# Optimization experiments

Hardware: AMD Instinct MI355X
Metric: run time of the kernel (lower is better)

Reference implementation:

```python
import jax, jax.numpy as jnp
import numpy as np
from jax import lax

B, T, D, H = 64, 2048, 128, 256

def _lstm_layer(x, Wih, Whh, bih, bhh):
    # x: [B, T, in]; Wih: [4H, in]; Whh: [4H, H]
    xp = jnp.einsum('bti,gi->btg', x, Wih) + bih + bhh  # [B, T, 4H]
    h0 = jnp.zeros((x.shape[0], Whh.shape[1]), x.dtype)
    c0 = jnp.zeros_like(h0)
    def step(carry, xt):
        h, c = carry
        g = xt + h @ Whh.T
        i, f, gg, o = jnp.split(g, 4, axis=-1)
        c = jax.nn.sigmoid(f) * c + jax.nn.sigmoid(i) * jnp.tanh(gg)
        h = jax.nn.sigmoid(o) * jnp.tanh(c)
        return (h, c), h
    _, hs = lax.scan(step, (h0, c0), jnp.swapaxes(xp, 0, 1))  # hs: [T, B, H]
    return jnp.swapaxes(hs, 0, 1)

def setup_inputs() -> dict:
    key = jax.random.key(0)
    ks = jax.random.split(key, 16)
    s_ih0 = 1.0 / np.sqrt(H)
    inp = {
        'x': jax.random.normal(ks[0], (B, T, D), jnp.float32),
        'Wih0': jax.random.uniform(ks[1], (4 * H, D), jnp.float32, -s_ih0, s_ih0),
        'Whh0': jax.random.uniform(ks[2], (4 * H, H), jnp.float32, -s_ih0, s_ih0),
        'bih0': jax.random.uniform(ks[3], (4 * H,), jnp.float32, -s_ih0, s_ih0),
        'bhh0': jax.random.uniform(ks[4], (4 * H,), jnp.float32, -s_ih0, s_ih0),
        'Wih1': jax.random.uniform(ks[5], (4 * H, H), jnp.float32, -s_ih0, s_ih0),
        'Whh1': jax.random.uniform(ks[6], (4 * H, H), jnp.float32, -s_ih0, s_ih0),
        'bih1': jax.random.uniform(ks[7], (4 * H,), jnp.float32, -s_ih0, s_ih0),
        'bhh1': jax.random.uniform(ks[8], (4 * H,), jnp.float32, -s_ih0, s_ih0),
        'attn_W1': jax.random.normal(ks[9], (H, H), jnp.float32) * np.sqrt(2.0 / (H + H)),
        'attn_W2': jax.random.normal(ks[10], (H, H), jnp.float32) * np.sqrt(2.0 / (H + H)),
        'attn_w': jax.random.uniform(ks[11], (H,), jnp.float32, -0.1, 0.1),
        'ln_gamma': jnp.ones((H,), jnp.float32),
        'ln_beta': jnp.zeros((H,), jnp.float32),
    }
    return inp

def reference(x, Wih0, Whh0, bih0, bhh0, Wih1, Whh1, bih1, bhh1, attn_W1, attn_W2, attn_w, ln_gamma, ln_beta):
    h1 = _lstm_layer(x, Wih0, Whh0, bih0, bhh0)       # [B, T, H]
    lstm_out = _lstm_layer(h1, Wih1, Whh1, bih1, bhh1)  # [B, T, H]
    h_T = lstm_out[:, -1, :]                            # [B, H]
    # vectorized additive attention over all timesteps
    alpha = jnp.tanh(jnp.einsum('bth,hk->btk', lstm_out, attn_W1)
                     + (h_T @ attn_W2)[:, None, :])     # [B, T, H]
    scores = alpha @ attn_w                             # [B, T]
    w = jax.nn.softmax(scores, axis=1)
    context = jnp.einsum('bt,bth->bh', w, lstm_out)     # [B, H]
    mu = jnp.mean(context, axis=-1, keepdims=True)
    var = jnp.var(context, axis=-1, keepdims=True)
    out = (context - mu) / jnp.sqrt(var + 1e-5) * ln_gamma + ln_beta
    return out
```

## Files before the change

### kernel.cpp

```cpp
#include <hip/hip_runtime.h>
#include <hip/hip_bf16.h>
#include <math.h>

#define B 64
#define T 2048
#define D 128
#define H 256
#define G 1024

#define L0_UINTS 49152
#define L1_UINTS 65536
#define PQ_UINTS (L0_UINTS + L1_UINTS)

#define L0_RES 22
#define L1_RES 20
#define L0_LDS 2
#define L1_LDS 12

typedef _Float16 h2v __attribute__((ext_vector_type(2)));
typedef float f2v __attribute__((ext_vector_type(2)));
typedef unsigned int u4v __attribute__((ext_vector_type(4)));

#if defined(__has_builtin)
#if __has_builtin(__builtin_amdgcn_fdot2)
#define HAS_FDOT2 1
#endif
#endif

__device__ __forceinline__ float dot2(unsigned int w, unsigned int h, float acc) {
#ifdef HAS_FDOT2
    return __builtin_amdgcn_fdot2(__builtin_bit_cast(h2v, w), __builtin_bit_cast(h2v, h), acc, false);
#else
    h2v wv = __builtin_bit_cast(h2v, w);
    h2v hv = __builtin_bit_cast(h2v, h);
    acc = fmaf((float)wv.x, (float)hv.x, acc);
    return fmaf((float)wv.y, (float)hv.y, acc);
#endif
}

__device__ __forceinline__ unsigned short f2h(float f) {
    _Float16 h = (_Float16)f;
    return __builtin_bit_cast(unsigned short, h);
}
__device__ __forceinline__ float h2f(unsigned short u) {
    return (float)__builtin_bit_cast(_Float16, u);
}
__device__ __forceinline__ unsigned int packh2(float a, float b) {
    return (unsigned int)f2h(a) | ((unsigned int)f2h(b) << 16);
}
__device__ __forceinline__ float sigm(float x) { return 1.0f / (1.0f + __expf(-x)); }
__device__ __forceinline__ float ftanh(float x) {
    x = fminf(fmaxf(x, -15.0f), 15.0f);
    float e = __expf(2.0f * x);
    return (e - 1.0f) / (e + 1.0f);
}

#define DOT4(w0, hp, a0, a1, a2, a3) \
    a0 = dot2(w0.x, hp, a0); a1 = dot2(w0.y, hp, a1); a2 = dot2(w0.z, hp, a2); a3 = dot2(w0.w, hp, a3);

__global__ void k_zero(unsigned int* p, int n) {
    int i = blockIdx.x * blockDim.x + threadIdx.x;
    if (i < n) p[i] = 0u;
}

__global__ void k_bias_sum(const float* __restrict__ a, const float* __restrict__ b,
                           float* __restrict__ out, int n) {
    int i = blockIdx.x * blockDim.x + threadIdx.x;
    if (i < n) out[i] = a[i] + b[i];
}

__global__ void k_pack_w(const float* __restrict__ Wih0, const float* __restrict__ Whh0,
                         const float* __restrict__ Wih1, const float* __restrict__ Whh1,
                         unsigned int* __restrict__ PW) {
    int idx = blockIdx.x * blockDim.x + threadIdx.x;
    if (idx >= 4 * PQ_UINTS) return;
    int q = idx / PQ_UINTS;
    int off = idx % PQ_UINTS;
    float v0, v1;
    if (off < L0_UINTS) {
        int kp = off >> 8, c = off & 255;
        int gate = c >> 6, u = c & 63;
        int r = gate * 256 + q * 64 + u;
        int k = kp * 2;
        if (k < 128) { v0 = Wih0[(size_t)r * 128 + k];       v1 = Wih0[(size_t)r * 128 + k + 1]; }
        else         { v0 = Whh0[(size_t)r * 256 + k - 128]; v1 = Whh0[(size_t)r * 256 + k - 127]; }
    } else {
        int o2 = off - L0_UINTS;
        int kp = o2 >> 8, c = o2 & 255;
        int gate = c >> 6, u = c & 63;
        int r = gate * 256 + q * 64 + u;
        int k = kp * 2;
        if (k < 256) { v0 = Wih1[(size_t)r * 256 + k];       v1 = Wih1[(size_t)r * 256 + k + 1]; }
        else         { v0 = Whh1[(size_t)r * 256 + k - 256]; v1 = Whh1[(size_t)r * 256 + k - 255]; }
    }
    PW[idx] = packh2(v0, v1);
}

__global__ __launch_bounds__(1024, 4) void k_lstm_split(
    const float* __restrict__ x,
    const unsigned int* __restrict__ PW,
    const float* __restrict__ bs0,
    const float* __restrict__ bs1,
    unsigned int* __restrict__ hxq,
    unsigned int* __restrict__ flags,
    unsigned int* __restrict__ seqo)
{
    __shared__ float s_gacc[8][512];
    __shared__ float s_g[512];
    __shared__ unsigned int s_k0p[192];
    __shared__ unsigned int s_k1p[256];
    __shared__ uint4 wl0[L0_LDS][512];
    __shared__ uint4 wl1[L1_LDS][512];

    const int q   = blockIdx.x >> 6;
    const int b   = blockIdx.x & 63;
    const int tid = threadIdx.x;
    const int half = tid >> 9;
    const int t2  = tid & 511;
    const int cg  = t2 & 63;
    const int kb  = t2 >> 6;

    const unsigned int* Wq = PW + (size_t)q * PQ_UINTS;
    const unsigned int* wbase =
        half == 0 ? (Wq + (size_t)(kb * 24) * 256 + 4 * cg)
                  : (Wq + L0_UINTS + (size_t)(kb * 32) * 256 + 4 * cg);

    uint4 wr[L0_RES];
    if (half == 0) {
        #pragma unroll
        for (int i = 0; i < L0_RES; ++i) wr[i] = *(const uint4*)(wbase + (size_t)i * 256);
        #pragma unroll
        for (int c = 0; c < L0_LDS; ++c)
            wl0[c][t2] = *(const uint4*)(wbase + (size_t)(L0_RES + c) * 256);
    } else {
        #pragma unroll
        for (int i = 0; i < L1_RES; ++i) wr[i] = *(const uint4*)(wbase + (size_t)i * 256);
        #pragma unroll
        for (int c = 0; c < L1_LDS; ++c)
            wl1[c][t2] = *(const uint4*)(wbase + (size_t)(L1_RES + c) * 256);
    }

    float bi0 = 0.f, bi1 = 0.f, bi2 = 0.f, bi3 = 0.f;
    if (tid < 64) {
        int u = q * 64 + tid;
        bi0 = bs0[u]; bi1 = bs0[256 + u]; bi2 = bs0[512 + u]; bi3 = bs0[768 + u];
    } else if (tid < 128) {
        int u = q * 64 + (tid - 64);
        bi0 = bs1[u]; bi1 = bs1[256 + u]; bi2 = bs1[512 + u]; bi3 = bs1[768 + u];
    }
    float c0 = 0.f, c1 = 0.f;
    unsigned int hb0 = 0u, hb1 = 0u, hb2 = 0u, hb3 = 0u;

    if (tid < 128) s_k0p[64 + tid] = 0u;
    if (tid >= 128 && tid < 384) s_k1p[tid - 128] = 0u;
    if (tid >= 384 && tid < 448) {
        int i = tid - 384;
        f2v v = __builtin_nontemporal_load((const f2v*)(x + (size_t)b * T * D) + i);
        s_k0p[i] = packh2(v.x, v.y);
    }

    for (int t = 0; ; ++t) {
        __syncthreads();

        if (half == 0) {
            if (t < T) {
                const unsigned int* sp = s_k0p + kb * 24;
                float a0 = 0.f, a1 = 0.f, a2 = 0.f, a3 = 0.f;
                #pragma unroll
                for (int i = 0; i < 5; ++i) {
                    uint4 hp = *(const uint4*)(sp + 4 * i);
                    DOT4(wr[4 * i + 0], hp.x, a0, a1, a2, a3);
                    DOT4(wr[4 * i + 1], hp.y, a0, a1, a2, a3);
                    DOT4(wr[4 * i + 2], hp.z, a0, a1, a2, a3);
                    DOT4(wr[4 * i + 3], hp.w, a0, a1, a2, a3);
                }
                {
                    uint4 hp = *(const uint4*)(sp + 20);
                    DOT4(wr[20], hp.x, a0, a1, a2, a3);
                    DOT4(wr[21], hp.y, a0, a1, a2, a3);
                    uint4 wa = wl0[0][t2];
                    DOT4(wa, hp.z, a0, a1, a2, a3);
                    uint4 wb = wl0[1][t2];
                    DOT4(wb, hp.w, a0, a1, a2, a3);
                }
                *(float4*)&s_gacc[kb][4 * cg] = make_float4(a0, a1, a2, a3);
            }
        } else {
            const unsigned int* sp = s_k1p + kb * 32;
            float a0 = 0.f, a1 = 0.f, a2 = 0.f, a3 = 0.f;
            #pragma unroll
            for (int i = 0; i < 5; ++i) {
                uint4 hp = *(const uint4*)(sp + 4 * i);
                DOT4(wr[4 * i + 0], hp.x, a0, a1, a2, a3);
                DOT4(wr[4 * i + 1], hp.y, a0, a1, a2, a3);
                DOT4(wr[4 * i + 2], hp.z, a0, a1, a2, a3);
                DOT4(wr[4 * i + 3], hp.w, a0, a1, a2, a3);
            }
            #pragma unroll
            for (int g = 0; g < 3; ++g) {
                uint4 hp = *(const uint4*)(sp + 20 + 4 * g);
                uint4 w0 = wl1[4 * g + 0][t2];
                DOT4(w0, hp.x, a0, a1, a2, a3);
                uint4 w1 = wl1[4 * g + 1][t2];
                DOT4(w1, hp.y, a0, a1, a2, a3);
                uint4 w2 = wl1[4 * g + 2][t2];
                DOT4(w2, hp.z, a0, a1, a2, a3);
                uint4 w3 = wl1[4 * g + 3][t2];
                DOT4(w3, hp.w, a0, a1, a2, a3);
            }
            *(float4*)&s_gacc[kb][256 + 4 * cg] = make_float4(a0, a1, a2, a3);
        }
        __syncthreads();

        if (tid < 512) {
            float s = s_gacc[0][tid] + s_gacc[1][tid] + s_gacc[2][tid] + s_gacc[3][tid]
                    + s_gacc[4][tid] + s_gacc[5][tid] + s_gacc[6][tid] + s_gacc[7][tid];
            s_g[tid] = s;
        }
        __syncthreads();

        if (tid < 64) {
            if (t < T) {
                int u = tid;
                float gi = s_g[u] + bi0;
                float gf = s_g[64 + u] + bi1;
                float gg = s_g[128 + u] + bi2;
                float go = s_g[192 + u] + bi3;
                c0 = sigm(gf) * c0 + sigm(gi) * ftanh(gg);
                float h0v = sigm(go) * ftanh(c0);
                float other = __shfl_xor(h0v, 1);
                if ((u & 1) == 0) {
                    __hip_atomic_store(hxq + ((((size_t)(t & 1) * 4 + q) * 64 + b) * 64) + (u >> 1),
                                       packh2(h0v, other), __ATOMIC_RELAXED, __HIP_MEMORY_SCOPE_AGENT);
                }
            }
        } else if (tid < 128) {
            int u = tid - 64;
            float h1v = 0.0f;
            if (t >= 1) {
                float gi = s_g[256 + u] + bi0;
                float gf = s_g[320 + u] + bi1;
                float gg = s_g[384 + u] + bi2;
                float go = s_g[448 + u] + bi3;
                c1 = sigm(gf) * c1 + sigm(gi) * ftanh(gg);
                h1v = sigm(go) * ftanh(c1);
                unsigned int hv = (unsigned int)f2h(h1v);
                int s = (t - 1) & 7;
                switch (s) {
                    case 0: hb0 = hv; break;
                    case 1: hb0 |= hv << 16; break;
                    case 2: hb1 = hv; break;
                    case 3: hb1 |= hv << 16; break;
                    case 4: hb2 = hv; break;
                    case 5: hb2 |= hv << 16; break;
                    case 6: hb3 = hv; break;
                    default: hb3 |= hv << 16; break;
                }
                if (s == 7) {
                    size_t idx = ((size_t)b * (T / 8) + ((t - 1) >> 3)) * H + (q * 64 + u);
                    u4v val = {hb0, hb1, hb2, hb3};
                    __builtin_nontemporal_store(val, (u4v*)(seqo + idx * 4));
                }
            }
            if (t < T) {
                float other = __shfl_xor(h1v, 1);
                if ((u & 1) == 0) {
                    __hip_atomic_store(hxq + ((((size_t)(t & 1) * 4 + q) * 64 + b) * 64) + 32 + (u >> 1),
                                       packh2(h1v, other), __ATOMIC_RELAXED, __HIP_MEMORY_SCOPE_AGENT);
                }
            }
        }

        if (t == T) break;

        __syncthreads();

        if (tid == 0) {
            __hip_atomic_store(flags + ((size_t)q * 64 + b) * 64, (unsigned)(t + 1),
                               __ATOMIC_RELAXED, __HIP_MEMORY_SCOPE_AGENT);
        }

        {
            const int wv = tid >> 6, l = tid & 63;
            if (wv < 4) {
                unsigned f = 0;
                const unsigned int* fp = flags + ((size_t)wv * 64 + b) * 64;
                do {
                    if (l == 0) f = __hip_atomic_load(fp, __ATOMIC_RELAXED, __HIP_MEMORY_SCOPE_AGENT);
                    f = __shfl(f, 0);
                    if (f < (unsigned)(t + 1)) __builtin_amdgcn_s_sleep(1);
                } while (f < (unsigned)(t + 1));
                unsigned v = __hip_atomic_load(
                    hxq + ((((size_t)(t & 1) * 4 + wv) * 64 + b) * 64) + l,
                    __ATOMIC_RELAXED, __HIP_MEMORY_SCOPE_AGENT);
                if (l < 32) {
                    s_k0p[64 + wv * 32 + l] = v;
                    s_k1p[wv * 32 + l] = v;
                } else {
                    s_k1p[128 + wv * 32 + (l - 32)] = v;
                }
            } else if (wv == 4) {
                if (t + 1 < T) {
                    f2v v = __builtin_nontemporal_load(
                        (const f2v*)(x + ((size_t)b * T + (t + 1)) * D) + l);
                    s_k0p[l] = packh2(v.x, v.y);
                }
            }
        }
    }
}

__global__ __launch_bounds__(256) void k_a2(const unsigned int* __restrict__ seq,
                                            const float* __restrict__ W2,
                                            float* __restrict__ a2out)
{
    __shared__ float s_hT[H];
    int b = blockIdx.x;
    int k = threadIdx.x;
    unsigned v = seq[(((size_t)b * (T / 8) + 255) * H + k) * 4 + 3];
    s_hT[k] = h2f((unsigned short)(v >> 16));
    __syncthreads();
    float acc = 0.f;
    #pragma unroll 4
    for (int h = 0; h < H; ++h) acc += s_hT[h] * W2[h * H + k];
    a2out[b * H + k] = acc;
}

__global__ __launch_bounds__(256) void k_scores(const unsigned int* __restrict__ seq,
                                                const float* __restrict__ W1,
                                                const float* __restrict__ a2,
                                                const float* __restrict__ attn_w,
                                                float* __restrict__ scores)
{
    const int RPB = 32;
    __shared__ float s_rows[RPB][H];
    __shared__ float s_part[RPB][4];
    int b   = blockIdx.y;
    int t0  = blockIdx.x * RPB;
    int tid = threadIdx.x;

    for (int it = tid; it < 4 * H; it += 256) {
        int tgi = it >> 8, h = it & 255;
        uint4 v = ((const uint4*)seq)[((size_t)b * (T / 8) + (t0 >> 3) + tgi) * H + h];
        int r0 = tgi * 8;
        s_rows[r0 + 0][h] = h2f((unsigned short)v.x);
        s_rows[r0 + 1][h] = h2f((unsigned short)(v.x >> 16));
        s_rows[r0 + 2][h] = h2f((unsigned short)v.y);
        s_rows[r0 + 3][h] = h2f((unsigned short)(v.y >> 16));
        s_rows[r0 + 4][h] = h2f((unsigned short)v.z);
        s_rows[r0 + 5][h] = h2f((unsigned short)(v.z >> 16));
        s_rows[r0 + 6][h] = h2f((unsigned short)v.w);
        s_rows[r0 + 7][h] = h2f((unsigned short)(v.w >> 16));
    }
    __syncthreads();

    int c = tid;
    float acc[RPB];
    #pragma unroll
    for (int r = 0; r < RPB; ++r) acc[r] = 0.f;
    for (int h = 0; h < H; ++h) {
        float w = W1[h * H + c];
        #pragma unroll
        for (int r = 0; r < RPB; ++r) acc[r] += s_rows[r][h] * w;
    }
    float a2v = a2[b * H + c];
    float wc  = attn_w[c];
    int lane = tid & 63, wv = tid >> 6;
    #pragma unroll
    for (int r = 0; r < RPB; ++r) {
        float v = ftanh(acc[r] + a2v) * wc;
        for (int off = 32; off; off >>= 1) v += __shfl_down(v, off);
        if (lane == 0) s_part[r][wv] = v;
    }
    __syncthreads();
    if (tid < RPB) {
        scores[(size_t)b * T + t0 + tid] =
            s_part[tid][0] + s_part[tid][1] + s_part[tid][2] + s_part[tid][3];
    }
}

__global__ __launch_bounds__(256) void k_finish(const unsigned int* __restrict__ seq,
                                                const float* __restrict__ scores,
                                                const float* __restrict__ gamma,
                                                const float* __restrict__ beta,
                                                float* __restrict__ out)
{
    __shared__ float s_p[T];
    __shared__ float s_red[4];
    const int b = blockIdx.x;
    const int tid = threadIdx.x;
    const int lane = tid & 63, wv = tid >> 6;

    const float* sc = scores + (size_t)b * T;
    float m = -1e30f;
    for (int t = tid; t < T; t += 256) m = fmaxf(m, sc[t]);
    for (int off = 32; off; off >>= 1) m = fmaxf(m, __shfl_down(m, off));
    if (lane == 0) s_red[wv] = m;
    __syncthreads();
    m = fmaxf(fmaxf(s_red[0], s_red[1]), fmaxf(s_red[2], s_red[3]));
    __syncthreads();

    float z = 0.f;
    for (int t = tid; t < T; t += 256) { float e = __expf(sc[t] - m); s_p[t] = e; z += e; }
    for (int off = 32; off; off >>= 1) z += __shfl_down(z, off);
    if (lane == 0) s_red[wv] = z;
    __syncthreads();
    z = s_red[0] + s_red[1] + s_red[2] + s_red[3];
    float rz = 1.0f / z;
    __syncthreads();

    const uint4* sq = (const uint4*)seq + (size_t)b * (T / 8) * H + tid;
    float ctx = 0.f;
    for (int tg = 0; tg < T / 8; ++tg) {
        uint4 v = sq[(size_t)tg * H];
        const float* pp = &s_p[tg * 8];
        ctx += pp[0] * h2f((unsigned short)v.x) + pp[1] * h2f((unsigned short)(v.x >> 16))
             + pp[2] * h2f((unsigned short)v.y) + pp[3] * h2f((unsigned short)(v.y >> 16))
             + pp[4] * h2f((unsigned short)v.z) + pp[5] * h2f((unsigned short)(v.z >> 16))
             + pp[6] * h2f((unsigned short)v.w) + pp[7] * h2f((unsigned short)(v.w >> 16));
    }
    ctx *= rz;

    float s1 = ctx;
    for (int off = 32; off; off >>= 1) s1 += __shfl_down(s1, off);
    if (lane == 0) s_red[wv] = s1;
    __syncthreads();
    float mu = (s_red[0] + s_red[1] + s_red[2] + s_red[3]) * (1.0f / H);
    __syncthreads();
    float dv = ctx - mu;
    float s2 = dv * dv;
    for (int off = 32; off; off >>= 1) s2 += __shfl_down(s2, off);
    if (lane == 0) s_red[wv] = s2;
    __syncthreads();
    float var = (s_red[0] + s_red[1] + s_red[2] + s_red[3]) * (1.0f / H);
    out[b * H + tid] = dv * rsqrtf(var + 1e-5f) * gamma[tid] + beta[tid];
}

extern "C" void kernel_launch(void* const* d_in, const int* in_sizes, int n_in,
                              void* d_out, int out_size, void* d_ws, size_t ws_size,
                              hipStream_t stream) {
    const float* x     = (const float*)d_in[0];
    const float* Wih0  = (const float*)d_in[1];
    const float* Whh0  = (const float*)d_in[2];
    const float* bih0  = (const float*)d_in[3];
    const float* bhh0  = (const float*)d_in[4];
    const float* Wih1  = (const float*)d_in[5];
    const float* Whh1  = (const float*)d_in[6];
    const float* bih1  = (const float*)d_in[7];
    const float* bhh1  = (const float*)d_in[8];
    const float* aW1   = (const float*)d_in[9];
    const float* aW2   = (const float*)d_in[10];
    const float* aw    = (const float*)d_in[11];
    const float* gamma = (const float*)d_in[12];
    const float* beta  = (const float*)d_in[13];
    float* out = (float*)d_out;

    char* base = (char*)d_ws;
    unsigned int* PW    = (unsigned int*)(base);
    float* bsum0        = (float*)(base + 1835008);
    float* bsum1        = (float*)(base + 1839104);
    unsigned int* flags = (unsigned int*)(base + 1843200);
    unsigned int* hxq   = (unsigned int*)(base + 1908736);
    float* a2buf        = (float*)(base + 2039808);
    float* scoresb      = (float*)(base + 2105344);
    unsigned int* seqo  = (unsigned int*)(base + 2629632);

    k_zero<<<(4 * 64 * 64 + 255) / 256, 256, 0, stream>>>(flags, 4 * 64 * 64);
    k_pack_w<<<(4 * PQ_UINTS) / 256, 256, 0, stream>>>(Wih0, Whh0, Wih1, Whh1, PW);
    k_bias_sum<<<(G + 255) / 256, 256, 0, stream>>>(bih0, bhh0, bsum0, G);
    k_bias_sum<<<(G + 255) / 256, 256, 0, stream>>>(bih1, bhh1, bsum1, G);

    k_lstm_split<<<256, 1024, 0, stream>>>(x, PW, bsum0, bsum1, hxq, flags, seqo);

    k_a2<<<B, H, 0, stream>>>(seqo, aW2, a2buf);
    k_scores<<<dim3(T / 32, B), 256, 0, stream>>>(seqo, aW1, a2buf, aw, scoresb);
    k_finish<<<B, 256, 0, stream>>>(seqo, scoresb, gamma, beta, out);
}
```

Measured before the change: 8.200 ms.

## Repartition persistent LSTM across 16 hidden slices times 16 batch groups

The persistent two-layer LSTM kernel changes its work split. Each block used to own a 64-unit quarter of the hidden state for one batch row. Now each block owns a 16-unit slice for a group of 4 batch rows, so every weight element loaded from LDS is reused across 4 batches. All of a slice's weights now live in LDS instead of per-thread registers, and partial sums are reduced with cross-lane shuffles. Each block now waits on 16 peer flags per step instead of 4, which adds inter-block synchronisation traffic in exchange for less register pressure and better weight reuse.

```diff
diff --git a/kernel.cpp b/kernel.cpp
--- a/kernel.cpp
+++ b/kernel.cpp
@@ -8,14 +8,13 @@
 #define H 256
 #define G 1024
 
-#define L0_UINTS 49152
-#define L1_UINTS 65536
-#define PQ_UINTS (L0_UINTS + L1_UINTS)
-
-#define L0_RES 22
-#define L1_RES 20
-#define L0_LDS 2
-#define L1_LDS 12
+#define NSL 16
+#define NB 4
+#define NG 16
+#define L0_U4 3072
+#define L1_U4 4096
+#define SL_U4 (L0_U4 + L1_U4)
+#define SL_UINTS (SL_U4 * 4)
 
 typedef _Float16 h2v __attribute__((ext_vector_type(2)));
 typedef float f2v __attribute__((ext_vector_type(2)));
@@ -55,8 +54,15 @@
     return (e - 1.0f) / (e + 1.0f);
 }
 
-#define DOT4(w0, hp, a0, a1, a2, a3) \
-    a0 = dot2(w0.x, hp, a0); a1 = dot2(w0.y, hp, a1); a2 = dot2(w0.z, hp, a2); a3 = dot2(w0.w, hp, a3);
+#define DOTB(w_, h_) \
+    A0.x=dot2(w_.x,h_.x,A0.x); A0.y=dot2(w_.x,h_.y,A0.y); A0.z=dot2(w_.x,h_.z,A0.z); A0.w=dot2(w_.x,h_.w,A0.w); \
+    A1.x=dot2(w_.y,h_.x,A1.x); A1.y=dot2(w_.y,h_.y,A1.y); A1.z=dot2(w_.y,h_.z,A1.z); A1.w=dot2(w_.y,h_.w,A1.w); \
+    A2.x=dot2(w_.z,h_.x,A2.x); A2.y=dot2(w_.z,h_.y,A2.y); A2.z=dot2(w_.z,h_.z,A2.z); A2.w=dot2(w_.z,h_.w,A2.w); \
+    A3.x=dot2(w_.w,h_.x,A3.x); A3.y=dot2(w_.w,h_.y,A3.y); A3.z=dot2(w_.w,h_.z,A3.z); A3.w=dot2(w_.w,h_.w,A3.w);
+
+#define RED4(A) \
+    A.x += __shfl_xor(A.x, 16); A.y += __shfl_xor(A.y, 16); A.z += __shfl_xor(A.z, 16); A.w += __shfl_xor(A.w, 16); \
+    A.x += __shfl_xor(A.x, 32); A.y += __shfl_xor(A.y, 32); A.z += __shfl_xor(A.z, 32); A.w += __shfl_xor(A.w, 32);
 
 __global__ void k_zero(unsigned int* p, int n) {
     int i = blockIdx.x * blockDim.x + threadIdx.x;
@@ -73,180 +79,158 @@
                          const float* __restrict__ Wih1, const float* __restrict__ Whh1,
                          unsigned int* __restrict__ PW) {
     int idx = blockIdx.x * blockDim.x + threadIdx.x;
-    if (idx >= 4 * PQ_UINTS) return;
-    int q = idx / PQ_UINTS;
-    int off = idx % PQ_UINTS;
+    if (idx >= NSL * SL_UINTS) return;
+    int s = idx / SL_UINTS;
+    int rem = idx % SL_UINTS;
     float v0, v1;
-    if (off < L0_UINTS) {
-        int kp = off >> 8, c = off & 255;
-        int gate = c >> 6, u = c & 63;
-        int r = gate * 256 + q * 64 + u;
-        int k = kp * 2;
-        if (k < 128) { v0 = Wih0[(size_t)r * 128 + k];       v1 = Wih0[(size_t)r * 128 + k + 1]; }
-        else         { v0 = Whh0[(size_t)r * 256 + k - 128]; v1 = Whh0[(size_t)r * 256 + k - 127]; }
+    if (rem < L0_U4 * 4) {
+        int q4 = rem >> 2, e = rem & 3;
+        int kb = q4 / 96; int r = q4 % 96; int kp = r >> 4; int cg = r & 15;
+        int c = cg * 4 + e; int g4 = c >> 4; int u = c & 15;
+        int row = g4 * 256 + s * 16 + u;
+        int k = (kb * 6 + kp) * 2;
+        if (k < 128) { v0 = Wih0[(size_t)row * 128 + k];         v1 = Wih0[(size_t)row * 128 + k + 1]; }
+        else         { v0 = Whh0[(size_t)row * 256 + (k - 128)]; v1 = Whh0[(size_t)row * 256 + (k - 127)]; }
     } else {
-        int o2 = off - L0_UINTS;
-        int kp = o2 >> 8, c = o2 & 255;
-        int gate = c >> 6, u = c & 63;
-        int r = gate * 256 + q * 64 + u;
-        int k = kp * 2;
-        if (k < 256) { v0 = Wih1[(size_t)r * 256 + k];       v1 = Wih1[(size_t)r * 256 + k + 1]; }
-        else         { v0 = Whh1[(size_t)r * 256 + k - 256]; v1 = Whh1[(size_t)r * 256 + k - 255]; }
+        int rem2 = rem - L0_U4 * 4;
+        int q4 = rem2 >> 2, e = rem2 & 3;
+        int kb = q4 / 128; int r = q4 % 128; int kp = r >> 4; int cg = r & 15;
+        int c = cg * 4 + e; int g4 = c >> 4; int u = c & 15;
+        int row = g4 * 256 + s * 16 + u;
+        int k = (kb * 8 + kp) * 2;
+        if (k < 256) { v0 = Wih1[(size_t)row * 256 + k];         v1 = Wih1[(size_t)row * 256 + k + 1]; }
+        else         { v0 = Whh1[(size_t)row * 256 + (k - 256)]; v1 = Whh1[(size_t)row * 256 + (k - 255)]; }
     }
     PW[idx] = packh2(v0, v1);
 }
 
-__global__ __launch_bounds__(1024, 4) void k_lstm_split(
+__global__ __launch_bounds__(1024) void k_lstm_split(
     const float* __restrict__ x,
-    const unsigned int* __restrict__ PW,
+    const uint4* __restrict__ PW2,
     const float* __restrict__ bs0,
     const float* __restrict__ bs1,
-    unsigned int* __restrict__ hxq,
+    unsigned int* __restrict__ hxg,
     unsigned int* __restrict__ flags,
     unsigned int* __restrict__ seqo)
 {
+    __shared__ uint4 wl[SL_U4];
     __shared__ float s_gacc[8][512];
     __shared__ float s_g[512];
-    __shared__ unsigned int s_k0p[192];
-    __shared__ unsigned int s_k1p[256];
-    __shared__ uint4 wl0[L0_LDS][512];
-    __shared__ uint4 wl1[L1_LDS][512];
-
-    const int q   = blockIdx.x >> 6;
-    const int b   = blockIdx.x & 63;
+    __shared__ unsigned int s_k0p[768];
+    __shared__ unsigned int s_k1p[1024];
+
+    const int g   = blockIdx.x & 15;
+    const int s   = blockIdx.x >> 4;
     const int tid = threadIdx.x;
-    const int half = tid >> 9;
-    const int t2  = tid & 511;
-    const int cg  = t2 & 63;
-    const int kb  = t2 >> 6;
-
-    const unsigned int* Wq = PW + (size_t)q * PQ_UINTS;
-    const unsigned int* wbase =
-        half == 0 ? (Wq + (size_t)(kb * 24) * 256 + 4 * cg)
-                  : (Wq + L0_UINTS + (size_t)(kb * 32) * 256 + 4 * cg);
-
-    uint4 wr[L0_RES];
-    if (half == 0) {
-        #pragma unroll
-        for (int i = 0; i < L0_RES; ++i) wr[i] = *(const uint4*)(wbase + (size_t)i * 256);
-        #pragma unroll
-        for (int c = 0; c < L0_LDS; ++c)
-            wl0[c][t2] = *(const uint4*)(wbase + (size_t)(L0_RES + c) * 256);
-    } else {
-        #pragma unroll
-        for (int i = 0; i < L1_RES; ++i) wr[i] = *(const uint4*)(wbase + (size_t)i * 256);
-        #pragma unroll
-        for (int c = 0; c < L1_LDS; ++c)
-            wl1[c][t2] = *(const uint4*)(wbase + (size_t)(L1_RES + c) * 256);
+    const int lane = tid & 63;
+    const int wv   = tid >> 6;
+    const int cg   = lane & 15;
+    const int kbs  = lane >> 4;
+
+    {
+        const uint4* PWs = PW2 + (size_t)s * SL_U4;
+        for (int i = tid; i < SL_U4; i += 1024) wl[i] = PWs[i];
     }
 
     float bi0 = 0.f, bi1 = 0.f, bi2 = 0.f, bi3 = 0.f;
     if (tid < 64) {
-        int u = q * 64 + tid;
-        bi0 = bs0[u]; bi1 = bs0[256 + u]; bi2 = bs0[512 + u]; bi3 = bs0[768 + u];
+        int u = tid >> 2;
+        bi0 = bs0[s * 16 + u]; bi1 = bs0[256 + s * 16 + u];
+        bi2 = bs0[512 + s * 16 + u]; bi3 = bs0[768 + s * 16 + u];
     } else if (tid < 128) {
-        int u = q * 64 + (tid - 64);
-        bi0 = bs1[u]; bi1 = bs1[256 + u]; bi2 = bs1[512 + u]; bi3 = bs1[768 + u];
+        int u = (tid - 64) >> 2;
+        bi0 = bs1[s * 16 + u]; bi1 = bs1[256 + s * 16 + u];
+        bi2 = bs1[512 + s * 16 + u]; bi3 = bs1[768 + s * 16 + u];
     }
     float c0 = 0.f, c1 = 0.f;
     unsigned int hb0 = 0u, hb1 = 0u, hb2 = 0u, hb3 = 0u;
 
-    if (tid < 128) s_k0p[64 + tid] = 0u;
-    if (tid >= 128 && tid < 384) s_k1p[tid - 128] = 0u;
-    if (tid >= 384 && tid < 448) {
-        int i = tid - 384;
-        f2v v = __builtin_nontemporal_load((const f2v*)(x + (size_t)b * T * D) + i);
-        s_k0p[i] = packh2(v.x, v.y);
+    if (tid < 512) s_k0p[256 + tid] = 0u;
+    s_k1p[tid] = 0u;
+    if (tid >= 512 && tid < 768) {
+        int i = tid - 512; int b = i >> 6; int kp = i & 63;
+        f2v v = __builtin_nontemporal_load((const f2v*)(x + (size_t)(g * NB + b) * T * D) + kp);
+        s_k0p[kp * 4 + b] = packh2(v.x, v.y);
     }
 
     for (int t = 0; ; ++t) {
         __syncthreads();
 
-        if (half == 0) {
+        if (wv < 8) {
             if (t < T) {
-                const unsigned int* sp = s_k0p + kb * 24;
-                float a0 = 0.f, a1 = 0.f, a2 = 0.f, a3 = 0.f;
+                int kb = wv * 4 + kbs;
+                const uint4* wp = wl + (size_t)(kb * 6) * 16 + cg;
+                float4 A0 = make_float4(0.f,0.f,0.f,0.f), A1 = A0, A2 = A0, A3 = A0;
                 #pragma unroll
-                for (int i = 0; i < 5; ++i) {
-                    uint4 hp = *(const uint4*)(sp + 4 * i);
-                    DOT4(wr[4 * i + 0], hp.x, a0, a1, a2, a3);
-                    DOT4(wr[4 * i + 1], hp.y, a0, a1, a2, a3);
-                    DOT4(wr[4 * i + 2], hp.z, a0, a1, a2, a3);
-                    DOT4(wr[4 * i + 3], hp.w, a0, a1, a2, a3);
-                }
-                {
-                    uint4 hp = *(const uint4*)(sp + 20);
-                    DOT4(wr[20], hp.x, a0, a1, a2, a3);
-                    DOT4(wr[21], hp.y, a0, a1, a2, a3);
-                    uint4 wa = wl0[0][t2];
-                    DOT4(wa, hp.z, a0, a1, a2, a3);
-                    uint4 wb = wl0[1][t2];
-                    DOT4(wb, hp.w, a0, a1, a2, a3);
-                }
-                *(float4*)&s_gacc[kb][4 * cg] = make_float4(a0, a1, a2, a3);
+                for (int kp = 0; kp < 6; ++kp) {
+                    uint4 w = wp[kp * 16];
+                    uint4 h = *(const uint4*)&s_k0p[(kb * 6 + kp) * 4];
+                    DOTB(w, h);
+                }
+                RED4(A0); RED4(A1); RED4(A2); RED4(A3);
+                if (kbs == 0) {
+                    *(float4*)&s_gacc[wv][cg * 16 + 0]  = A0;
+                    *(float4*)&s_gacc[wv][cg * 16 + 4]  = A1;
+                    *(float4*)&s_gacc[wv][cg * 16 + 8]  = A2;
+                    *(float4*)&s_gacc[wv][cg * 16 + 12] = A3;
+                }
             }
         } else {
-            const unsigned int* sp = s_k1p + kb * 32;
-            float a0 = 0.f, a1 = 0.f, a2 = 0.f, a3 = 0.f;
+            int kb = (wv - 8) * 4 + kbs;
+            const uint4* wp = wl + L0_U4 + (size_t)(kb * 8) * 16 + cg;
+            float4 A0 = make_float4(0.f,0.f,0.f,0.f), A1 = A0, A2 = A0, A3 = A0;
             #pragma unroll
-            for (int i = 0; i < 5; ++i) {
-                uint4 hp = *(const uint4*)(sp + 4 * i);
-                DOT4(wr[4 * i + 0], hp.x, a0, a1, a2, a3);
-                DOT4(wr[4 * i + 1], hp.y, a0, a1, a2, a3);
-                DOT4(wr[4 * i + 2], hp.z, a0, a1, a2, a3);
-                DOT4(wr[4 * i + 3], hp.w, a0, a1, a2, a3);
-            }
-            #pragma unroll
-            for (int g = 0; g < 3; ++g) {
-                uint4 hp = *(const uint4*)(sp + 20 + 4 * g);
-                uint4 w0 = wl1[4 * g + 0][t2];
-                DOT4(w0, hp.x, a0, a1, a2, a3);
-                uint4 w1 = wl1[4 * g + 1][t2];
-                DOT4(w1, hp.y, a0, a1, a2, a3);
-                uint4 w2 = wl1[4 * g + 2][t2];
-                DOT4(w2, hp.z, a0, a1, a2, a3);
-                uint4 w3 = wl1[4 * g + 3][t2];
-                DOT4(w3, hp.w, a0, a1, a2, a3);
-            }
-            *(float4*)&s_gacc[kb][256 + 4 * cg] = make_float4(a0, a1, a2, a3);
+            for (int kp = 0; kp < 8; ++kp) {
+                uint4 w = wp[kp * 16];
+                uint4 h = *(const uint4*)&s_k1p[(kb * 8 + kp) * 4];
+                DOTB(w, h);
+            }
+            RED4(A0); RED4(A1); RED4(A2); RED4(A3);
+            if (kbs == 0) {
+                *(float4*)&s_gacc[wv - 8][256 + cg * 16 + 0]  = A0;
+                *(float4*)&s_gacc[wv - 8][256 + cg * 16 + 4]  = A1;
+                *(float4*)&s_gacc[wv - 8][256 + cg * 16 + 8]  = A2;
+                *(float4*)&s_gacc[wv - 8][256 + cg * 16 + 12] = A3;
+            }
         }
         __syncthreads();
 
         if (tid < 512) {
-            float s = s_gacc[0][tid] + s_gacc[1][tid] + s_gacc[2][tid] + s_gacc[3][tid]
-                    + s_gacc[4][tid] + s_gacc[5][tid] + s_gacc[6][tid] + s_gacc[7][tid];
-            s_g[tid] = s;
+            float sum = s_gacc[0][tid] + s_gacc[1][tid] + s_gacc[2][tid] + s_gacc[3][tid]
+                      + s_gacc[4][tid] + s_gacc[5][tid] + s_gacc[6][tid] + s_gacc[7][tid];
+            s_g[tid] = sum;
         }
         __syncthreads();
 
         if (tid < 64) {
             if (t < T) {
-                int u = tid;
-                float gi = s_g[u] + bi0;
-                float gf = s_g[64 + u] + bi1;
-                float gg = s_g[128 + u] + bi2;
-                float go = s_g[192 + u] + bi3;
+                int u = tid >> 2, b = tid & 3;
+                float gi = s_g[u * 4 + b]          + bi0;
+                float gf = s_g[(16 + u) * 4 + b]   + bi1;
+                float gg = s_g[(32 + u) * 4 + b]   + bi2;
+                float go = s_g[(48 + u) * 4 + b]   + bi3;
                 c0 = sigm(gf) * c0 + sigm(gi) * ftanh(gg);
                 float h0v = sigm(go) * ftanh(c0);
-                float other = __shfl_xor(h0v, 1);
+                float other = __shfl_xor(h0v, 4);
                 if ((u & 1) == 0) {
-                    __hip_atomic_store(hxq + ((((size_t)(t & 1) * 4 + q) * 64 + b) * 64) + (u >> 1),
-                                       packh2(h0v, other), __ATOMIC_RELAXED, __HIP_MEMORY_SCOPE_AGENT);
+                    size_t off = (((size_t)(t & 1) * NG + g) * NSL + s) * 64 + (u >> 1) * 4 + b;
+                    __hip_atomic_store(hxg + off, packh2(h0v, other),
+                                       __ATOMIC_RELAXED, __HIP_MEMORY_SCOPE_AGENT);
                 }
             }
         } else if (tid < 128) {
-            int u = tid - 64;
+            int u = (tid - 64) >> 2, b = tid & 3;
             float h1v = 0.0f;
             if (t >= 1) {
-                float gi = s_g[256 + u] + bi0;
-                float gf = s_g[320 + u] + bi1;
-                float gg = s_g[384 + u] + bi2;
-                float go = s_g[448 + u] + bi3;
+                float gi = s_g[256 + u * 4 + b]        + bi0;
+                float gf = s_g[256 + (16 + u) * 4 + b] + bi1;
+                float gg = s_g[256 + (32 + u) * 4 + b] + bi2;
+                float go = s_g[256 + (48 + u) * 4 + b] + bi3;
                 c1 = sigm(gf) * c1 + sigm(gi) * ftanh(gg);
                 h1v = sigm(go) * ftanh(c1);
                 unsigned int hv = (unsigned int)f2h(h1v);
-                int s = (t - 1) & 7;
-                switch (s) {
+                int st = (t - 1) & 7;
+                switch (st) {
                     case 0: hb0 = hv; break;
                     case 1: hb0 |= hv << 16; break;
                     case 2: hb1 = hv; break;
@@ -256,18 +240,26 @@
                     case 6: hb3 = hv; break;
                     default: hb3 |= hv << 16; break;
                 }
-                if (s == 7) {
-                    size_t idx = ((size_t)b * (T / 8) + ((t - 1) >> 3)) * H + (q * 64 + u);
+                if (st == 7) {
+                    size_t idx = ((size_t)(g * NB + b) * (T / 8) + ((t - 1) >> 3)) * H + (s * 16 + u);
                     u4v val = {hb0, hb1, hb2, hb3};
                     __builtin_nontemporal_store(val, (u4v*)(seqo + idx * 4));
                 }
             }
             if (t < T) {
-                float other = __shfl_xor(h1v, 1);
+                float other = __shfl_xor(h1v, 4);
                 if ((u & 1) == 0) {
-                    __hip_atomic_store(hxq + ((((size_t)(t & 1) * 4 + q) * 64 + b) * 64) + 32 + (u >> 1),
-                                       packh2(h1v, other), __ATOMIC_RELAXED, __HIP_MEMORY_SCOPE_AGENT);
-                }
+                    size_t off = (((size_t)(t & 1) * NG + g) * NSL + s) * 64 + 32 + (u >> 1) * 4 + b;
+                    __hip_atomic_store(hxg + off, packh2(h1v, other),
+                                       __ATOMIC_RELAXED, __HIP_MEMORY_SCOPE_AGENT);
+                }
+            }
+        } else if (tid >= 512 && tid < 768) {
+            if (t + 1 < T) {
+                int i = tid - 512; int b = i >> 6; int kp = i & 63;
+                f2v v = __builtin_nontemporal_load(
+                    (const f2v*)(x + (size_t)(g * NB + b) * T * D) + (size_t)(t + 1) * 64 + kp);
+                s_k0p[kp * 4 + b] = packh2(v.x, v.y);
             }
         }
 
@@ -276,35 +268,28 @@
         __syncthreads();
 
         if (tid == 0) {
-            __hip_atomic_store(flags + ((size_t)q * 64 + b) * 64, (unsigned)(t + 1),
+            __hip_atomic_store(flags + ((size_t)g * NSL + s) * 64, (unsigned)(t + 1),
                                __ATOMIC_RELAXED, __HIP_MEMORY_SCOPE_AGENT);
         }
 
         {
-            const int wv = tid >> 6, l = tid & 63;
-            if (wv < 4) {
-                unsigned f = 0;
-                const unsigned int* fp = flags + ((size_t)wv * 64 + b) * 64;
-                do {
-                    if (l == 0) f = __hip_atomic_load(fp, __ATOMIC_RELAXED, __HIP_MEMORY_SCOPE_AGENT);
-                    f = __shfl(f, 0);
-                    if (f < (unsigned)(t + 1)) __builtin_amdgcn_s_sleep(1);
-                } while (f < (unsigned)(t + 1));
-                unsigned v = __hip_atomic_load(
-                    hxq + ((((size_t)(t & 1) * 4 + wv) * 64 + b) * 64) + l,
-                    __ATOMIC_RELAXED, __HIP_MEMORY_SCOPE_AGENT);
-                if (l < 32) {
-                    s_k0p[64 + wv * 32 + l] = v;
-                    s_k1p[wv * 32 + l] = v;
-                } else {
-                    s_k1p[128 + wv * 32 + (l - 32)] = v;
-                }
-            } else if (wv == 4) {
-                if (t + 1 < T) {
-                    f2v v = __builtin_nontemporal_load(
-                        (const f2v*)(x + ((size_t)b * T + (t + 1)) * D) + l);
-                    s_k0p[l] = packh2(v.x, v.y);
-                }
+            unsigned f = 0;
+            const unsigned int* fp = flags + ((size_t)g * NSL + wv) * 64;
+            do {
+                if (lane == 0) f = __hip_atomic_load(fp, __ATOMIC_RELAXED, __HIP_MEMORY_SCOPE_AGENT);
+                f = __shfl(f, 0);
+                if (f < (unsigned)(t + 1)) __builtin_amdgcn_s_sleep(1);
+            } while (f < (unsigned)(t + 1));
+            unsigned v = __hip_atomic_load(
+                hxg + (((size_t)(t & 1) * NG + g) * NSL + wv) * 64 + lane,
+                __ATOMIC_RELAXED, __HIP_MEMORY_SCOPE_AGENT);
+            int layer = lane >> 5, kp_loc = (lane >> 2) & 7, b = lane & 3;
+            int kpg = wv * 8 + kp_loc;
+            if (layer == 0) {
+                s_k0p[(64 + kpg) * 4 + b] = v;
+                s_k1p[kpg * 4 + b] = v;
+            } else {
+                s_k1p[(128 + kpg) * 4 + b] = v;
             }
         }
     }
@@ -460,17 +445,17 @@
     float* bsum0        = (float*)(base + 1835008);
     float* bsum1        = (float*)(base + 1839104);
     unsigned int* flags = (unsigned int*)(base + 1843200);
-    unsigned int* hxq   = (unsigned int*)(base + 1908736);
+    unsigned int* hxg   = (unsigned int*)(base + 1908736);
     float* a2buf        = (float*)(base + 2039808);
     float* scoresb      = (float*)(base + 2105344);
     unsigned int* seqo  = (unsigned int*)(base + 2629632);
 
-    k_zero<<<(4 * 64 * 64 + 255) / 256, 256, 0, stream>>>(flags, 4 * 64 * 64);
-    k_pack_w<<<(4 * PQ_UINTS) / 256, 256, 0, stream>>>(Wih0, Whh0, Wih1, Whh1, PW);
+    k_zero<<<(NG * NSL * 64 + 255) / 256, 256, 0, stream>>>(flags, NG * NSL * 64);
+    k_pack_w<<<(NSL * SL_UINTS) / 256, 256, 0, stream>>>(Wih0, Whh0, Wih1, Whh1, PW);
     k_bias_sum<<<(G + 255) / 256, 256, 0, stream>>>(bih0, bhh0, bsum0, G);
     k_bias_sum<<<(G + 255) / 256, 256, 0, stream>>>(bih1, bhh1, bsum1, G);
 
-    k_lstm_split<<<256, 1024, 0, stream>>>(x, PW, bsum0, bsum1, hxq, flags, seqo);
+    k_lstm_split<<<256, 1024, 0, stream>>>(x, (const uint4*)PW, bsum0, bsum1, hxg, flags, seqo);
 
     k_a2<<<B, H, 0, stream>>>(seqo, aW2, a2buf);
     k_scores<<<dim3(T / 32, B), 256, 0, stream>>>(seqo, aW1, a2buf, aw, scoresb);
```

Measured after the change: 9.180 ms. 1.12x slower.

## Fuse step tags into hidden-state words and stream weights from global memory

Applied to the files above, without the earlier changes.

Each exchanged hidden-state word now carries its timestep in the upper 32 bits of a 64-bit store. Consumers poll the data directly until every lane sees the right tag, which removes the separate flag store, the extra block barrier and the flag round-trip. Register-resident weights are dropped: most weights are reloaded from global memory each step and a few more go into LDS. This lowers register pressure but adds per-step global/L2 traffic. The next x row is also prefetched into a register at the start of the step.

```diff
diff --git a/kernel.cpp b/kernel.cpp
--- a/kernel.cpp
+++ b/kernel.cpp
@@ -12,10 +12,8 @@
 #define L1_UINTS 65536
 #define PQ_UINTS (L0_UINTS + L1_UINTS)
 
-#define L0_RES 22
-#define L1_RES 20
-#define L0_LDS 2
-#define L1_LDS 12
+#define L0_LDS 3
+#define L1_LDS 14
 
 typedef _Float16 h2v __attribute__((ext_vector_type(2)));
 typedef float f2v __attribute__((ext_vector_type(2)));
@@ -96,13 +94,12 @@
     PW[idx] = packh2(v0, v1);
 }
 
-__global__ __launch_bounds__(1024, 4) void k_lstm_split(
+__global__ __launch_bounds__(1024) void k_lstm_split(
     const float* __restrict__ x,
     const unsigned int* __restrict__ PW,
     const float* __restrict__ bs0,
     const float* __restrict__ bs1,
-    unsigned int* __restrict__ hxq,
-    unsigned int* __restrict__ flags,
+    unsigned long long* __restrict__ hx64,
     unsigned int* __restrict__ seqo)
 {
     __shared__ float s_gacc[8][512];
@@ -125,19 +122,14 @@
         half == 0 ? (Wq + (size_t)(kb * 24) * 256 + 4 * cg)
                   : (Wq + L0_UINTS + (size_t)(kb * 32) * 256 + 4 * cg);
 
-    uint4 wr[L0_RES];
     if (half == 0) {
         #pragma unroll
-        for (int i = 0; i < L0_RES; ++i) wr[i] = *(const uint4*)(wbase + (size_t)i * 256);
-        #pragma unroll
         for (int c = 0; c < L0_LDS; ++c)
-            wl0[c][t2] = *(const uint4*)(wbase + (size_t)(L0_RES + c) * 256);
+            wl0[c][t2] = *(const uint4*)(wbase + (size_t)(21 + c) * 256);
     } else {
         #pragma unroll
-        for (int i = 0; i < L1_RES; ++i) wr[i] = *(const uint4*)(wbase + (size_t)i * 256);
-        #pragma unroll
         for (int c = 0; c < L1_LDS; ++c)
-            wl1[c][t2] = *(const uint4*)(wbase + (size_t)(L1_RES + c) * 256);
+            wl1[c][t2] = *(const uint4*)(wbase + (size_t)(18 + c) * 256);
     }
 
     float bi0 = 0.f, bi1 = 0.f, bi2 = 0.f, bi3 = 0.f;
@@ -150,6 +142,7 @@
     }
     float c0 = 0.f, c1 = 0.f;
     unsigned int hb0 = 0u, hb1 = 0u, hb2 = 0u, hb3 = 0u;
+    f2v xr = {0.f, 0.f};
 
     if (tid < 128) s_k0p[64 + tid] = 0u;
     if (tid >= 128 && tid < 384) s_k1p[tid - 128] = 0u;
@@ -161,6 +154,11 @@
 
     for (int t = 0; ; ++t) {
         __syncthreads();
+
+        if ((tid >> 6) == 4 && (t + 1) < T) {
+            xr = __builtin_nontemporal_load(
+                (const f2v*)(x + ((size_t)b * T + (t + 1)) * D) + (tid & 63));
+        }
 
         if (half == 0) {
             if (t < T) {
@@ -169,19 +167,25 @@
                 #pragma unroll
                 for (int i = 0; i < 5; ++i) {
                     uint4 hp = *(const uint4*)(sp + 4 * i);
-                    DOT4(wr[4 * i + 0], hp.x, a0, a1, a2, a3);
-                    DOT4(wr[4 * i + 1], hp.y, a0, a1, a2, a3);
-                    DOT4(wr[4 * i + 2], hp.z, a0, a1, a2, a3);
-                    DOT4(wr[4 * i + 3], hp.w, a0, a1, a2, a3);
+                    uint4 w0 = *(const uint4*)(wbase + (size_t)(4 * i + 0) * 256);
+                    uint4 w1 = *(const uint4*)(wbase + (size_t)(4 * i + 1) * 256);
+                    uint4 w2 = *(const uint4*)(wbase + (size_t)(4 * i + 2) * 256);
+                    uint4 w3 = *(const uint4*)(wbase + (size_t)(4 * i + 3) * 256);
+                    DOT4(w0, hp.x, a0, a1, a2, a3);
+                    DOT4(w1, hp.y, a0, a1, a2, a3);
+                    DOT4(w2, hp.z, a0, a1, a2, a3);
+                    DOT4(w3, hp.w, a0, a1, a2, a3);
                 }
                 {
                     uint4 hp = *(const uint4*)(sp + 20);
-                    DOT4(wr[20], hp.x, a0, a1, a2, a3);
-                    DOT4(wr[21], hp.y, a0, a1, a2, a3);
+                    uint4 w20 = *(const uint4*)(wbase + (size_t)20 * 256);
+                    DOT4(w20, hp.x, a0, a1, a2, a3);
                     uint4 wa = wl0[0][t2];
-                    DOT4(wa, hp.z, a0, a1, a2, a3);
+                    DOT4(wa, hp.y, a0, a1, a2, a3);
                     uint4 wb = wl0[1][t2];
-                    DOT4(wb, hp.w, a0, a1, a2, a3);
+                    DOT4(wb, hp.z, a0, a1, a2, a3);
+                    uint4 wc = wl0[2][t2];
+                    DOT4(wc, hp.w, a0, a1, a2, a3);
                 }
                 *(float4*)&s_gacc[kb][4 * cg] = make_float4(a0, a1, a2, a3);
             }
@@ -189,23 +193,38 @@
             const unsigned int* sp = s_k1p + kb * 32;
             float a0 = 0.f, a1 = 0.f, a2 = 0.f, a3 = 0.f;
             #pragma unroll
-            for (int i = 0; i < 5; ++i) {
+            for (int i = 0; i < 4; ++i) {
                 uint4 hp = *(const uint4*)(sp + 4 * i);
-                DOT4(wr[4 * i + 0], hp.x, a0, a1, a2, a3);
-                DOT4(wr[4 * i + 1], hp.y, a0, a1, a2, a3);
-                DOT4(wr[4 * i + 2], hp.z, a0, a1, a2, a3);
-                DOT4(wr[4 * i + 3], hp.w, a0, a1, a2, a3);
+                uint4 w0 = *(const uint4*)(wbase + (size_t)(4 * i + 0) * 256);
+                uint4 w1 = *(const uint4*)(wbase + (size_t)(4 * i + 1) * 256);
+                uint4 w2 = *(const uint4*)(wbase + (size_t)(4 * i + 2) * 256);
+                uint4 w3 = *(const uint4*)(wbase + (size_t)(4 * i + 3) * 256);
+                DOT4(w0, hp.x, a0, a1, a2, a3);
+                DOT4(w1, hp.y, a0, a1, a2, a3);
+                DOT4(w2, hp.z, a0, a1, a2, a3);
+                DOT4(w3, hp.w, a0, a1, a2, a3);
+            }
+            {
+                uint4 hp = *(const uint4*)(sp + 16);
+                uint4 w16 = *(const uint4*)(wbase + (size_t)16 * 256);
+                DOT4(w16, hp.x, a0, a1, a2, a3);
+                uint4 w17 = *(const uint4*)(wbase + (size_t)17 * 256);
+                DOT4(w17, hp.y, a0, a1, a2, a3);
+                uint4 wa = wl1[0][t2];
+                DOT4(wa, hp.z, a0, a1, a2, a3);
+                uint4 wb = wl1[1][t2];
+                DOT4(wb, hp.w, a0, a1, a2, a3);
             }
             #pragma unroll
-            for (int g = 0; g < 3; ++g) {
-                uint4 hp = *(const uint4*)(sp + 20 + 4 * g);
-                uint4 w0 = wl1[4 * g + 0][t2];
+            for (int g2 = 0; g2 < 3; ++g2) {
+                uint4 hp = *(const uint4*)(sp + 20 + 4 * g2);
+                uint4 w0 = wl1[2 + 4 * g2][t2];
                 DOT4(w0, hp.x, a0, a1, a2, a3);
-                uint4 w1 = wl1[4 * g + 1][t2];
+                uint4 w1 = wl1[3 + 4 * g2][t2];
                 DOT4(w1, hp.y, a0, a1, a2, a3);
-                uint4 w2 = wl1[4 * g + 2][t2];
+                uint4 w2 = wl1[4 + 4 * g2][t2];
                 DOT4(w2, hp.z, a0, a1, a2, a3);
-                uint4 w3 = wl1[4 * g + 3][t2];
+                uint4 w3 = wl1[5 + 4 * g2][t2];
                 DOT4(w3, hp.w, a0, a1, a2, a3);
             }
             *(float4*)&s_gacc[kb][256 + 4 * cg] = make_float4(a0, a1, a2, a3);
@@ -230,8 +249,10 @@
                 float h0v = sigm(go) * ftanh(c0);
                 float other = __shfl_xor(h0v, 1);
                 if ((u & 1) == 0) {
-                    __hip_atomic_store(hxq + ((((size_t)(t & 1) * 4 + q) * 64 + b) * 64) + (u >> 1),
-                                       packh2(h0v, other), __ATOMIC_RELAXED, __HIP_MEMORY_SCOPE_AGENT);
+                    size_t off = (((size_t)(t & 1) * 4 + q) * 64 + b) * 64 + (u >> 1);
+                    unsigned long long vv = ((unsigned long long)(unsigned)(t + 1) << 32)
+                                          | (unsigned long long)packh2(h0v, other);
+                    __hip_atomic_store(hx64 + off, vv, __ATOMIC_RELAXED, __HIP_MEMORY_SCOPE_AGENT);
                 }
             }
         } else if (tid < 128) {
@@ -244,9 +265,20 @@
                 float go = s_g[448 + u] + bi3;
                 c1 = sigm(gf) * c1 + sigm(gi) * ftanh(gg);
                 h1v = sigm(go) * ftanh(c1);
+            }
+            if (t < T) {
+                float other = __shfl_xor(h1v, 1);
+                if ((u & 1) == 0) {
+                    size_t off = (((size_t)(t & 1) * 4 + q) * 64 + b) * 64 + 32 + (u >> 1);
+                    unsigned long long vv = ((unsigned long long)(unsigned)(t + 1) << 32)
+                                          | (unsigned long long)packh2(h1v, other);
+                    __hip_atomic_store(hx64 + off, vv, __ATOMIC_RELAXED, __HIP_MEMORY_SCOPE_AGENT);
+                }
+            }
+            if (t >= 1) {
                 unsigned int hv = (unsigned int)f2h(h1v);
-                int s = (t - 1) & 7;
-                switch (s) {
+                int st = (t - 1) & 7;
+                switch (st) {
                     case 0: hb0 = hv; break;
                     case 1: hb0 |= hv << 16; break;
                     case 2: hb1 = hv; break;
@@ -256,55 +288,37 @@
                     case 6: hb3 = hv; break;
                     default: hb3 |= hv << 16; break;
                 }
-                if (s == 7) {
+                if (st == 7) {
                     size_t idx = ((size_t)b * (T / 8) + ((t - 1) >> 3)) * H + (q * 64 + u);
                     u4v val = {hb0, hb1, hb2, hb3};
                     __builtin_nontemporal_store(val, (u4v*)(seqo + idx * 4));
                 }
             }
-            if (t < T) {
-                float other = __shfl_xor(h1v, 1);
-                if ((u & 1) == 0) {
-                    __hip_atomic_store(hxq + ((((size_t)(t & 1) * 4 + q) * 64 + b) * 64) + 32 + (u >> 1),
-                                       packh2(h1v, other), __ATOMIC_RELAXED, __HIP_MEMORY_SCOPE_AGENT);
-                }
-            }
         }
 
         if (t == T) break;
 
-        __syncthreads();
-
-        if (tid == 0) {
-            __hip_atomic_store(flags + ((size_t)q * 64 + b) * 64, (unsigned)(t + 1),
-                               __ATOMIC_RELAXED, __HIP_MEMORY_SCOPE_AGENT);
-        }
-
         {
-            const int wv = tid >> 6, l = tid & 63;
-            if (wv < 4) {
-                unsigned f = 0;
-                const unsigned int* fp = flags + ((size_t)wv * 64 + b) * 64;
+            const int wvv = tid >> 6, l = tid & 63;
+            if (wvv < 4) {
+                const unsigned long long* hp =
+                    hx64 + (((size_t)(t & 1) * 4 + wvv) * 64 + b) * 64 + l;
+                unsigned data;
+                int ok;
                 do {
-                    if (l == 0) f = __hip_atomic_load(fp, __ATOMIC_RELAXED, __HIP_MEMORY_SCOPE_AGENT);
-                    f = __shfl(f, 0);
-                    if (f < (unsigned)(t + 1)) __builtin_amdgcn_s_sleep(1);
-                } while (f < (unsigned)(t + 1));
-                unsigned v = __hip_atomic_load(
-                    hxq + ((((size_t)(t & 1) * 4 + wv) * 64 + b) * 64) + l,
-                    __ATOMIC_RELAXED, __HIP_MEMORY_SCOPE_AGENT);
+                    unsigned long long vv = __hip_atomic_load(hp, __ATOMIC_RELAXED, __HIP_MEMORY_SCOPE_AGENT);
+                    data = (unsigned)vv;
+                    ok = ((unsigned)(vv >> 32) >= (unsigned)(t + 1));
+                    if (!__all(ok)) __builtin_amdgcn_s_sleep(1);
+                } while (!__all(ok));
                 if (l < 32) {
-                    s_k0p[64 + wv * 32 + l] = v;
-                    s_k1p[wv * 32 + l] = v;
+                    s_k0p[64 + wvv * 32 + l] = data;
+                    s_k1p[wvv * 32 + l] = data;
                 } else {
-                    s_k1p[128 + wv * 32 + (l - 32)] = v;
-                }
-            } else if (wv == 4) {
-                if (t + 1 < T) {
-                    f2v v = __builtin_nontemporal_load(
-                        (const f2v*)(x + ((size_t)b * T + (t + 1)) * D) + l);
-                    s_k0p[l] = packh2(v.x, v.y);
-                }
+                    s_k1p[128 + wvv * 32 + (l - 32)] = data;
+                }
+            } else if (wvv == 4 && (t + 1) < T) {
+                s_k0p[l] = packh2(xr.x, xr.y);
             }
         }
     }
@@ -456,21 +470,20 @@
     float* out = (float*)d_out;
 
     char* base = (char*)d_ws;
-    unsigned int* PW    = (unsigned int*)(base);
-    float* bsum0        = (float*)(base + 1835008);
-    float* bsum1        = (float*)(base + 1839104);
-    unsigned int* flags = (unsigned int*)(base + 1843200);
-    unsigned int* hxq   = (unsigned int*)(base + 1908736);
-    float* a2buf        = (float*)(base + 2039808);
-    float* scoresb      = (float*)(base + 2105344);
-    unsigned int* seqo  = (unsigned int*)(base + 2629632);
-
-    k_zero<<<(4 * 64 * 64 + 255) / 256, 256, 0, stream>>>(flags, 4 * 64 * 64);
+    unsigned int* PW        = (unsigned int*)(base);
+    float* bsum0            = (float*)(base + 1835008);
+    float* bsum1            = (float*)(base + 1839104);
+    unsigned long long* hx64 = (unsigned long long*)(base + 1843200);
+    float* a2buf            = (float*)(base + 2105344);
+    float* scoresb          = (float*)(base + 2170880);
+    unsigned int* seqo      = (unsigned int*)(base + 2695168);
+
+    k_zero<<<(65536 + 255) / 256, 256, 0, stream>>>((unsigned int*)hx64, 65536);
     k_pack_w<<<(4 * PQ_UINTS) / 256, 256, 0, stream>>>(Wih0, Whh0, Wih1, Whh1, PW);
     k_bias_sum<<<(G + 255) / 256, 256, 0, stream>>>(bih0, bhh0, bsum0, G);
     k_bias_sum<<<(G + 255) / 256, 256, 0, stream>>>(bih1, bhh1, bsum1, G);
 
-    k_lstm_split<<<256, 1024, 0, stream>>>(x, PW, bsum0, bsum1, hxq, flags, seqo);
+    k_lstm_split<<<256, 1024, 0, stream>>>(x, PW, bsum0, bsum1, hx64, seqo);
 
     k_a2<<<B, H, 0, stream>>>(seqo, aW2, a2buf);
     k_scores<<<dim3(T / 32, B), 256, 0, stream>>>(seqo, aW1, a2buf, aw, scoresb);
```

Result: slower. 9.927 ms (+21.1%).
